# Kernel tuning notes

Measured on AMD Instinct MI355X. Metric: run time of the kernel, lower is better.

## Reference

```python
import jax, jax.numpy as jnp
import numpy as np

SLOT_DIM, EMB_DIM, HID, ACT_DIM, NUM_ACT = 256, 256, 1024, 128, 1024
EPS_SAMPLE = 1e-6
EPS_LN = 1e-5


def setup_inputs() -> dict:
    key = jax.random.key(0)
    ks = jax.random.split(key, 12)
    B, N, S = 128, 32, 12
    s = 0.02
    return {
        "slots": jax.random.normal(ks[0], (B, N, S, SLOT_DIM), jnp.float32),
        "noise": jax.random.normal(ks[1], (B, N - 1, S, ACT_DIM), jnp.float32),
        "W1": jax.random.normal(ks[2], (SLOT_DIM, HID), jnp.float32) * s,
        "b1": jnp.zeros((HID,), jnp.float32),
        "ln_g": jnp.ones((HID,), jnp.float32),
        "ln_b": jnp.zeros((HID,), jnp.float32),
        "W2": jax.random.normal(ks[3], (HID, EMB_DIM), jnp.float32) * s,
        "b2": jnp.zeros((EMB_DIM,), jnp.float32),
        "Wm": jax.random.normal(ks[4], (EMB_DIM, ACT_DIM), jnp.float32) * s,
        "bm": jnp.zeros((ACT_DIM,), jnp.float32),
        "Wv": jax.random.normal(ks[5], (EMB_DIM, ACT_DIM), jnp.float32) * s,
        "bv": jnp.zeros((ACT_DIM,), jnp.float32),
        "codebook": jax.random.normal(ks[6], (NUM_ACT, ACT_DIM), jnp.float32) * s,
    }


def reference(slots, noise, W1, b1, ln_g, ln_b, W2, b2, Wm, bm, Wv, bv, codebook):
    sg = jax.lax.stop_gradient
    B, N, S, _ = slots.shape
    # per-slot MLP encoder: Linear -> ReLU -> LayerNorm -> Linear
    h = jax.nn.relu(jnp.einsum('bnsd,dh->bnsh', slots, W1) + b1)
    mu = h.mean(-1, keepdims=True)
    var = h.var(-1, keepdims=True)
    h = (h - mu) * jax.lax.rsqrt(var + EPS_LN) * ln_g + ln_b
    e = jnp.einsum('bnsh,he->bnse', h, W2) + b2  # (B,N,S,emb)
    # action distribution from consecutive frames
    mean_tok = jnp.einsum('bnse,ea->bnsa', e, Wm) + bm
    var_tok = jnp.abs(jnp.einsum('bnse,ea->bnsa', e, Wv) + bv)
    adm = mean_tok[:, 1:] - mean_tok[:, :-1]  # (B,N-1,S,A)
    adv = var_tok[:, 1:] + var_tok[:, :-1]
    action_dist = jnp.stack([adm, adv], axis=2)  # (B,N-1,2,S,A)
    # reparameterized sample
    z = noise * jnp.sqrt(adv + EPS_SAMPLE) + adm
    # VQ: nearest codebook entry via squared L2 distances
    zf = z.reshape(-1, ACT_DIM)  # (M,A)
    d = (jnp.sum(zf * zf, axis=1, keepdims=True)
         - 2.0 * zf @ codebook.T
         + jnp.sum(codebook * codebook, axis=1))  # (M,num_actions)
    idx = jnp.argmin(d, axis=1)  # (M,)
    q = codebook[idx].reshape(z.shape)
    quant_loss = jnp.mean((sg(z) - q) ** 2)
    commit_loss = jnp.mean((z - sg(q)) ** 2)
    q_st = z + sg(q - z)  # straight-through action prototypes
    action_variability = z - sg(q)
    action_idxs = idx.reshape(B, N - 1, S, 1)
    return (action_dist, z, action_variability, q_st, action_idxs, quant_loss, commit_loss)
```

## Files before the change

kernel.cpp:

```cpp
#include <hip/hip_runtime.h>
#include <math.h>

#define HID 1024
#define SLOT 256
#define EMB 256
#define ACT 128
#define NCODE 1024
#define R_ROWS 49152
#define M_ROWS 47616

#define OFF_AD 0
#define OFF_Z  12189696
#define OFF_AV 18284544
#define OFF_QS 24379392
#define OFF_IDX 30474240
#define OFF_QL 30521856
#define OFF_CL 30521857

typedef _Float16 f16x8 __attribute__((ext_vector_type(8)));
typedef float f32x4 __attribute__((ext_vector_type(4)));

__device__ __forceinline__ void pack_body(
    const float* __restrict__ W, _Float16* __restrict__ hi, _Float16* __restrict__ lo,
    int lgS, int N, int p, const float* __restrict__ scale)
{
    int j = p & 7;
    int l = (p >> 3) & 63;
    int q = p >> 9;
    int s = q & ((1 << lgS) - 1);
    int t = q >> lgS;
    int n = t * 16 + (l & 15);
    int k = s * 32 + ((l >> 4) << 3) + j;
    float x = W[(size_t)k * N + n];
    if (scale) x *= scale[k];
    _Float16 h = (_Float16)x;
    hi[p] = h;
    lo[p] = (_Float16)(x - (float)h);
}

__global__ __launch_bounds__(256) void k_packall(
    const float* __restrict__ W1, const float* __restrict__ W2,
    const float* __restrict__ Wm, const float* __restrict__ Wv,
    const float* __restrict__ CB, const float* __restrict__ ln_g,
    const float* __restrict__ ln_b, const float* __restrict__ b2,
    _Float16* __restrict__ W1h, _Float16* __restrict__ W1l,
    _Float16* __restrict__ W2h, _Float16* __restrict__ W2l,
    _Float16* __restrict__ Wmh, _Float16* __restrict__ Wml,
    _Float16* __restrict__ Wvh, _Float16* __restrict__ Wvl,
    _Float16* __restrict__ CBh, _Float16* __restrict__ CBl,
    float* __restrict__ cn, float* __restrict__ v0, float* __restrict__ v1,
    float* __restrict__ losss)
{
    const int bi = blockIdx.x;
    const int tid = threadIdx.x;
    if (bi == 0 && tid == 0) *losss = 0.f;

    if (bi < 1024) {
        pack_body(W1, W1h, W1l, 3, HID, bi * 256 + tid, (const float*)0);
    } else if (bi < 2048) {
        pack_body(W2, W2h, W2l, 5, EMB, (bi - 1024) * 256 + tid, ln_g);
    } else if (bi < 2176) {
        pack_body(Wm, Wmh, Wml, 3, ACT, (bi - 2048) * 256 + tid, (const float*)0);
    } else if (bi < 2304) {
        pack_body(Wv, Wvh, Wvl, 3, ACT, (bi - 2176) * 256 + tid, (const float*)0);
    } else if (bi < 2816) {
        int p = (bi - 2304) * 256 + tid;
        int j = p & 7;
        int l = (p >> 3) & 63;
        int q = p >> 9;
        int s = q & 7;
        int t = q >> 3;
        int n = t * 32 + (l & 31);
        int k = s * 16 + ((l >> 5) << 3) + j;
        float x = CB[(size_t)n * ACT + k];
        _Float16 h = (_Float16)x;
        CBh[p] = h;
        CBl[p] = (_Float16)(x - (float)h);
    } else if (bi < 2820) {
        int c = (bi - 2816) * 256 + tid;
        float s = 0.f;
        #pragma unroll
        for (int k = 0; k < ACT; k += 4) {
            float4 v = *(const float4*)&CB[(size_t)c * ACT + k];
            s += v.x*v.x + v.y*v.y + v.z*v.z + v.w*v.w;
        }
        cn[c] = s;
    } else {
        int n = tid;
        float a0 = 0.f, a1 = 0.f;
        for (int c = 0; c < HID; ++c) {
            float w2 = W2[(size_t)c * EMB + n];
            a1 = fmaf(ln_g[c], w2, a1);
            a0 = fmaf(ln_b[c], w2, a0);
        }
        v1[n] = a1;
        v0[n] = a0 + b2[n];
    }
}

__global__ __launch_bounds__(512, 4) void k_gemm1(
    const float* __restrict__ X, const float* __restrict__ b1,
    const _Float16* __restrict__ W1h, const _Float16* __restrict__ W1l,
    _Float16* __restrict__ GHh, _Float16* __restrict__ GHl,
    float* __restrict__ stats, int row0)
{
    __shared__ _Float16 sh[32768];

    const int tid = threadIdx.x;
    const int w = tid >> 6, l = tid & 63, lr = l & 15, lg = l >> 4;
    const int p = blockIdx.x & 15;
    const int rg = blockIdx.x >> 4;
    const int rowc = rg * 128;

    {
        const float4* s0 = (const float4*)(W1h + (size_t)p * 16384);
        const float4* s1 = (const float4*)(W1l + (size_t)p * 16384);
        float4* d = (float4*)sh;
        #pragma unroll
        for (int i = 0; i < 4; ++i) {
            d[tid + 512 * i] = s0[tid + 512 * i];
            d[2048 + tid + 512 * i] = s1[tid + 512 * i];
        }
    }

    f16x8 a0[8], a1[8];
    {
        const float* xrow = X + (size_t)(row0 + rowc + w * 16 + lr) * SLOT + lg * 8;
        #pragma unroll
        for (int s = 0; s < 8; ++s) {
            float4 xa = *(const float4*)(xrow + 32 * s);
            float4 xb = *(const float4*)(xrow + 32 * s + 4);
            float xv[8] = {xa.x, xa.y, xa.z, xa.w, xb.x, xb.y, xb.z, xb.w};
            #pragma unroll
            for (int e = 0; e < 8; ++e) {
                _Float16 h = (_Float16)xv[e];
                a0[s][e] = h;
                a1[s][e] = (_Float16)(xv[e] - (float)h);
            }
        }
    }
    __syncthreads();

    f32x4 acc[4];
    #pragma unroll
    for (int t = 0; t < 4; ++t) acc[t] = (f32x4){0.f, 0.f, 0.f, 0.f};

    #pragma unroll
    for (int s = 0; s < 8; ++s) {
        #pragma unroll
        for (int t = 0; t < 4; ++t) {
            f16x8 bh = *(const f16x8*)&sh[((t * 8 + s) * 64 + l) * 8];
            f16x8 bl = *(const f16x8*)&sh[16384 + ((t * 8 + s) * 64 + l) * 8];
            acc[t] = __builtin_amdgcn_mfma_f32_16x16x32_f16(a0[s], bh, acc[t], 0, 0, 0);
            acc[t] = __builtin_amdgcn_mfma_f32_16x16x32_f16(a0[s], bl, acc[t], 0, 0, 0);
            acc[t] = __builtin_amdgcn_mfma_f32_16x16x32_f16(a1[s], bh, acc[t], 0, 0, 0);
        }
    }

    #pragma unroll
    for (int t = 0; t < 4; ++t) {
        float bb = b1[p * 64 + t * 16 + lr];
        #pragma unroll
        for (int r = 0; r < 4; ++r) acc[t][r] = fmaxf(acc[t][r] + bb, 0.f);
    }

    {
        float sum[4] = {0,0,0,0}, sq[4] = {0,0,0,0};
        #pragma unroll
        for (int t = 0; t < 4; ++t)
            #pragma unroll
            for (int r = 0; r < 4; ++r) {
                float v = acc[t][r];
                sum[r] += v; sq[r] = fmaf(v, v, sq[r]);
            }
        #pragma unroll
        for (int off = 1; off < 16; off <<= 1)
            #pragma unroll
            for (int r = 0; r < 4; ++r) {
                sum[r] += __shfl_xor(sum[r], off, 64);
                sq[r]  += __shfl_xor(sq[r],  off, 64);
            }
        if (lr == 0) {
            #pragma unroll
            for (int r = 0; r < 4; ++r) {
                size_t grow = (size_t)row0 + rowc + w * 16 + lg * 4 + r;
                float2 st = {sum[r], sq[r]};
                *(float2*)&stats[((size_t)p * R_ROWS + grow) * 2] = st;
            }
        }
    }
    __syncthreads();

    #pragma unroll
    for (int t = 0; t < 4; ++t) {
        #pragma unroll
        for (int r = 0; r < 4; ++r) {
            int rowloc = w * 16 + lg * 4 + r;
            int col = t * 16 + lr;
            int cc = col >> 3, j = col & 7;
            int ad = rowloc * 64 + ((cc ^ (rowloc & 7)) << 3) + j;
            float v = acc[t][r];
            _Float16 h = (_Float16)v;
            sh[ad] = h;
            sh[8192 + ad] = (_Float16)(v - (float)h);
        }
    }
    __syncthreads();

    #pragma unroll
    for (int i = 0; i < 2; ++i) {
        int u = tid + 512 * i;
        int RTl = u >> 7;
        int Sl  = (u >> 6) & 1;
        int li  = u & 63;
        int row = RTl * 16 + (li & 15);
        int cc  = Sl * 4 + (li >> 4);
        int ad  = row * 64 + ((cc ^ (row & 7)) << 3);
        f16x8 vh = *(const f16x8*)&sh[ad];
        f16x8 vl = *(const f16x8*)&sh[8192 + ad];
        size_t RTg = (size_t)rg * 8 + RTl;
        size_t off = ((RTg * 32 + (2 * p + Sl)) * 64 + li) * 8;
        *(f16x8*)&GHh[off] = vh;
        *(f16x8*)&GHl[off] = vl;
    }
}

__global__ __launch_bounds__(512, 4) void k_gemm2(
    const _Float16* __restrict__ GHh, const _Float16* __restrict__ GHl,
    const _Float16* __restrict__ W2h, const _Float16* __restrict__ W2l,
    const _Float16* __restrict__ Wmh, const _Float16* __restrict__ Wml,
    const _Float16* __restrict__ Wvh, const _Float16* __restrict__ Wvl,
    const float* __restrict__ stats, const float* __restrict__ v0,
    const float* __restrict__ v1, const float* __restrict__ bm,
    const float* __restrict__ bv,
    float* __restrict__ MT, float* __restrict__ VT, int row0)
{
    __shared__ _Float16 sh[32768];
    __shared__ float mu_s[64], rs_s[64];

    const int tid = threadIdx.x;
    const int w = tid >> 6, l = tid & 63, lr = l & 15, lg = l >> 4;
    const int rb = blockIdx.x;
    const size_t grow0 = (size_t)row0 + rb * 64;

    if (tid < 64) {
        float s = 0.f, q = 0.f;
        #pragma unroll
        for (int pp = 0; pp < 16; ++pp) {
            float2 st = *(const float2*)&stats[((size_t)pp * R_ROWS + grow0 + tid) * 2];
            s += st.x; q += st.y;
        }
        float mu = s * (1.f / HID);
        float var = q * (1.f / HID) - mu * mu;
        mu_s[tid] = mu;
        rs_s[tid] = 1.f / sqrtf(var + 1e-5f);
    }

    float v0r[2], v1r[2];
    #pragma unroll
    for (int t = 0; t < 2; ++t) {
        int n = w * 32 + t * 16 + lr;
        v0r[t] = v0[n];
        v1r[t] = v1[n];
    }

    f32x4 acc[4][2];
    #pragma unroll
    for (int rt = 0; rt < 4; ++rt)
        #pragma unroll
        for (int t = 0; t < 2; ++t) acc[rt][t] = (f32x4){0.f, 0.f, 0.f, 0.f};

    for (int kp = 0; kp < 8; ++kp) {
        __syncthreads();
        #pragma unroll
        for (int i = 0; i < 4; ++i) {
            int u = tid + 512 * i;
            int arr = u >> 10;
            int ui = u & 1023;
            int RTl = ui >> 8;
            int rem = ui & 255;
            size_t gu = ((size_t)(rb * 4 + RTl) * 32 + kp * 4) * 64 + rem;
            const _Float16* src = arr ? GHl : GHh;
            *(f16x8*)&sh[(size_t)arr * 8192 + (size_t)ui * 8] = *(const f16x8*)&src[gu * 8];
        }
        __syncthreads();

        #pragma unroll
        for (int sl = 0; sl < 4; ++sl) {
            f16x8 bh[2], bl[2];
            #pragma unroll
            for (int t = 0; t < 2; ++t) {
                int tg = w * 2 + t;
                size_t o = ((size_t)(tg * 32 + kp * 4 + sl) * 64 + l) * 8;
                bh[t] = *(const f16x8*)&W2h[o];
                bl[t] = *(const f16x8*)&W2l[o];
            }
            #pragma unroll
            for (int rt = 0; rt < 4; ++rt) {
                f16x8 ah = *(const f16x8*)&sh[((rt * 4 + sl) * 64 + l) * 8];
                f16x8 al = *(const f16x8*)&sh[8192 + ((rt * 4 + sl) * 64 + l) * 8];
                #pragma unroll
                for (int t = 0; t < 2; ++t) {
                    acc[rt][t] = __builtin_amdgcn_mfma_f32_16x16x32_f16(ah, bh[t], acc[rt][t], 0, 0, 0);
                    acc[rt][t] = __builtin_amdgcn_mfma_f32_16x16x32_f16(ah, bl[t], acc[rt][t], 0, 0, 0);
                    acc[rt][t] = __builtin_amdgcn_mfma_f32_16x16x32_f16(al, bh[t], acc[rt][t], 0, 0, 0);
                }
            }
        }
    }
    __syncthreads();

    #pragma unroll
    for (int rt = 0; rt < 4; ++rt) {
        #pragma unroll
        for (int t = 0; t < 2; ++t) {
            int n = w * 32 + t * 16 + lr;
            int cc = n >> 3, j = n & 7;
            #pragma unroll
            for (int r = 0; r < 4; ++r) {
                int row = rt * 16 + lg * 4 + r;
                float mu = mu_s[row], rs = rs_s[row];
                float e = rs * acc[rt][t][r] - rs * mu * v1r[t] + v0r[t];
                _Float16 h = (_Float16)e;
                int ad = row * 256 + ((cc ^ (row & 7)) << 3) + j;
                sh[ad] = h;
                sh[16384 + ad] = (_Float16)(e - (float)h);
            }
        }
    }
    __syncthreads();

    const _Float16* WXh = (w < 4) ? Wmh : Wvh;
    const _Float16* WXl = (w < 4) ? Wml : Wvl;
    f32x4 acc3[4][2];
    #pragma unroll
    for (int rt = 0; rt < 4; ++rt)
        #pragma unroll
        for (int t = 0; t < 2; ++t) acc3[rt][t] = (f32x4){0.f, 0.f, 0.f, 0.f};

    #pragma unroll
    for (int s = 0; s < 8; ++s) {
        f16x8 bh[2], bl[2];
        #pragma unroll
        for (int t = 0; t < 2; ++t) {
            int tg = (w & 3) * 2 + t;
            size_t o = ((size_t)(tg * 8 + s) * 64 + l) * 8;
            bh[t] = *(const f16x8*)&WXh[o];
            bl[t] = *(const f16x8*)&WXl[o];
        }
        #pragma unroll
        for (int rt = 0; rt < 4; ++rt) {
            int row = rt * 16 + lr;
            int cc = s * 4 + lg;
            int ad = row * 256 + ((cc ^ (row & 7)) << 3);
            f16x8 ah = *(const f16x8*)&sh[ad];
            f16x8 al = *(const f16x8*)&sh[16384 + ad];
            #pragma unroll
            for (int t = 0; t < 2; ++t) {
                acc3[rt][t] = __builtin_amdgcn_mfma_f32_16x16x32_f16(ah, bh[t], acc3[rt][t], 0, 0, 0);
                acc3[rt][t] = __builtin_amdgcn_mfma_f32_16x16x32_f16(ah, bl[t], acc3[rt][t], 0, 0, 0);
                acc3[rt][t] = __builtin_amdgcn_mfma_f32_16x16x32_f16(al, bh[t], acc3[rt][t], 0, 0, 0);
            }
        }
    }

    #pragma unroll
    for (int rt = 0; rt < 4; ++rt) {
        #pragma unroll
        for (int t = 0; t < 2; ++t) {
            int a = (w & 3) * 32 + t * 16 + lr;
            float bx = (w < 4) ? bm[a] : bv[a];
            #pragma unroll
            for (int r = 0; r < 4; ++r) {
                size_t grow = grow0 + rt * 16 + lg * 4 + r;
                float vv = acc3[rt][t][r] + bx;
                if (w < 4) MT[grow * ACT + a] = vv;
                else       VT[grow * ACT + a] = fabsf(vv);
            }
        }
    }
}

__global__ __launch_bounds__(256, 3) void k_vq32(
    const float* __restrict__ MT, const float* __restrict__ VT,
    const float* __restrict__ noise,
    const _Float16* __restrict__ CBh, const _Float16* __restrict__ CBl,
    const float* __restrict__ cn, const float* __restrict__ CB,
    float* __restrict__ out, float* __restrict__ losss)
{
    typedef float f32x16 __attribute__((ext_vector_type(16)));
    __shared__ _Float16 Zh[32 * 128];
    __shared__ _Float16 Zl[32 * 128];
    __shared__ float pb[4][32];
    __shared__ int   pi[4][32];
    __shared__ int   idx_s[32];
    __shared__ float red[4];

    const int tid = threadIdx.x;
    const int rowbase = blockIdx.x * 32;
    const int a = tid & 127;
    const int rhalf = tid >> 7;
    const int ga = a >> 3, ja = a & 7;

    for (int g = 0; g < 2; ++g) {
        float m1v[8], m2v[8], v1v[8], v2v[8], nzv[8];
        #pragma unroll
        for (int i = 0; i < 8; ++i) {
            int row = g * 16 + 2 * i + rhalf;
            int m = rowbase + row;
            int b = m / 372;
            int r1 = m + 12 * b;
            int r2 = r1 + 12;
            m1v[i] = MT[(size_t)r1 * ACT + a];
            m2v[i] = MT[(size_t)r2 * ACT + a];
            v1v[i] = VT[(size_t)r1 * ACT + a];
            v2v[i] = VT[(size_t)r2 * ACT + a];
            nzv[i] = noise[(size_t)m * ACT + a];
        }
        #pragma unroll
        for (int i = 0; i < 8; ++i) {
            int row = g * 16 + 2 * i + rhalf;
            int m = rowbase + row;
            float adm = m2v[i] - m1v[i];
            float adv = v2v[i] + v1v[i];
            float z = nzv[i] * sqrtf(adv + 1e-6f) + adm;
            int np = m / 12, s = m - np * 12;
            out[OFF_AD + (size_t)(np * 24 + s) * ACT + a] = adm;
            out[OFF_AD + (size_t)(np * 24 + 12 + s) * ACT + a] = adv;
            out[OFF_Z + (size_t)m * ACT + a] = z;
            _Float16 h = (_Float16)z;
            int ad = row * 128 + (((ga ^ (row & 15))) << 3) + ja;
            Zh[ad] = h;
            Zl[ad] = (_Float16)(z - (float)h);
        }
    }
    __syncthreads();

    const int w = tid >> 6, l = tid & 63;
    const int col = l & 31, hw = l >> 5;

    float best[16];
    int bidx[16];
    #pragma unroll
    for (int r = 0; r < 16; ++r) { best[r] = 3.4e38f; bidx[r] = 0; }

    for (int cc2 = 0; cc2 < 2; ++cc2) {
        f32x16 acc[4];
        #pragma unroll
        for (int t = 0; t < 4; ++t)
            #pragma unroll
            for (int r = 0; r < 16; ++r) acc[t][r] = 0.f;

        #pragma unroll
        for (int s = 0; s < 8; ++s) {
            int ad = col * 128 + (((s * 2 + hw) ^ (col & 15)) << 3);
            f16x8 ah = *(const f16x8*)&Zh[ad];
            f16x8 al = *(const f16x8*)&Zl[ad];
            #pragma unroll
            for (int t = 0; t < 4; ++t) {
                int tg = w * 8 + cc2 * 4 + t;
                f16x8 bh = *(const f16x8*)(CBh + ((size_t)(tg * 8 + s) * 64 + l) * 8);
                f16x8 bl = *(const f16x8*)(CBl + ((size_t)(tg * 8 + s) * 64 + l) * 8);
                acc[t] = __builtin_amdgcn_mfma_f32_32x32x16_f16(ah, bh, acc[t], 0, 0, 0);
                acc[t] = __builtin_amdgcn_mfma_f32_32x32x16_f16(ah, bl, acc[t], 0, 0, 0);
                acc[t] = __builtin_amdgcn_mfma_f32_32x32x16_f16(al, bh, acc[t], 0, 0, 0);
            }
        }

        float cnv[4];
        #pragma unroll
        for (int t = 0; t < 4; ++t) cnv[t] = cn[(w * 8 + cc2 * 4 + t) * 32 + col];

        #pragma unroll
        for (int reg = 0; reg < 16; ++reg) {
            #pragma unroll
            for (int t = 0; t < 4; ++t) {
                float d = cnv[t] - 2.f * acc[t][reg];
                int gi = (w * 8 + cc2 * 4 + t) * 32 + col;
                if (d < best[reg]) { best[reg] = d; bidx[reg] = gi; }
            }
        }
    }

    #pragma unroll
    for (int reg = 0; reg < 16; ++reg) {
        float bv_ = best[reg];
        int bi_ = bidx[reg];
        #pragma unroll
        for (int off = 1; off < 32; off <<= 1) {
            float ov = __shfl_xor(bv_, off, 64);
            int   oi = __shfl_xor(bi_, off, 64);
            if (ov < bv_ || (ov == bv_ && oi < bi_)) { bv_ = ov; bi_ = oi; }
        }
        if (col == 0) {
            int mrow = (reg & 3) + 8 * (reg >> 2) + 4 * hw;
            pb[w][mrow] = bv_;
            pi[w][mrow] = bi_;
        }
    }
    __syncthreads();

    if (tid < 32) {
        float bb = pb[0][tid];
        int bi_ = pi[0][tid];
        #pragma unroll
        for (int w2 = 1; w2 < 4; ++w2) {
            float v = pb[w2][tid];
            int ii = pi[w2][tid];
            if (v < bb || (v == bb && ii < bi_)) { bb = v; bi_ = ii; }
        }
        idx_s[tid] = bi_;
        out[OFF_IDX + rowbase + tid] = (float)bi_;
    }
    __syncthreads();

    float ls = 0.f;
    for (int g = 0; g < 2; ++g) {
        int civ[8]; float zv[8], qv[8];
        #pragma unroll
        for (int i = 0; i < 8; ++i) {
            int row = g * 16 + 2 * i + rhalf;
            civ[i] = idx_s[row];
            int ad = row * 128 + (((ga ^ (row & 15))) << 3) + ja;
            zv[i] = (float)Zh[ad] + (float)Zl[ad];
        }
        #pragma unroll
        for (int i = 0; i < 8; ++i) qv[i] = CB[(size_t)civ[i] * ACT + a];
        #pragma unroll
        for (int i = 0; i < 8; ++i) {
            int row = g * 16 + 2 * i + rhalf;
            size_t m = (size_t)(rowbase + row);
            float diff = zv[i] - qv[i];
            out[OFF_QS + m * ACT + a] = zv[i] + (qv[i] - zv[i]);
            out[OFF_AV + m * ACT + a] = diff;
            ls = fmaf(diff, diff, ls);
        }
    }
    #pragma unroll
    for (int off = 32; off; off >>= 1) ls += __shfl_xor(ls, off, 64);
    if (l == 0) red[w] = ls;
    __syncthreads();
    if (tid == 0) atomicAdd(losss, red[0] + red[1] + red[2] + red[3]);
}

__global__ void k_losses(const float* __restrict__ losss, float* __restrict__ out)
{
    float v = *losss * (1.f / 6094848.f);
    out[OFF_QL] = v;
    out[OFF_CL] = v;
}

extern "C" void kernel_launch(void* const* d_in, const int* in_sizes, int n_in,
                              void* d_out, int out_size, void* d_ws, size_t ws_size,
                              hipStream_t stream)
{
    const float* slots = (const float*)d_in[0];
    const float* noise = (const float*)d_in[1];
    const float* W1    = (const float*)d_in[2];
    const float* b1    = (const float*)d_in[3];
    const float* ln_g  = (const float*)d_in[4];
    const float* ln_b  = (const float*)d_in[5];
    const float* W2    = (const float*)d_in[6];
    const float* b2    = (const float*)d_in[7];
    const float* Wm    = (const float*)d_in[8];
    const float* bm    = (const float*)d_in[9];
    const float* Wv    = (const float*)d_in[10];
    const float* bv    = (const float*)d_in[11];
    const float* CB    = (const float*)d_in[12];
    float* out = (float*)d_out;
    float* ws  = (float*)d_ws;

    size_t ws_floats = ws_size / 4;
    int nchunk = (ws_floats >= 41000000) ? 2 : 4;
    int RC = R_ROWS / nchunk;

    _Float16* GHh = (_Float16*)ws;
    _Float16* GHl = (_Float16*)(ws + (size_t)RC * 512);
    float* MT = ws + (size_t)RC * 1024;
    float* VT = MT + 6291456;
    float* wb = VT + 6291456;
    _Float16* W1h = (_Float16*)(wb + 0);
    _Float16* W1l = (_Float16*)(wb + 131072);
    _Float16* W2h = (_Float16*)(wb + 262144);
    _Float16* W2l = (_Float16*)(wb + 393216);
    _Float16* Wmh = (_Float16*)(wb + 524288);
    _Float16* Wml = (_Float16*)(wb + 540672);
    _Float16* Wvh = (_Float16*)(wb + 557056);
    _Float16* Wvl = (_Float16*)(wb + 573440);
    _Float16* CBh = (_Float16*)(wb + 589824);
    _Float16* CBl = (_Float16*)(wb + 655360);
    float* cn    = wb + 720896;
    float* v0    = wb + 721920;
    float* v1    = wb + 722176;
    float* losss = wb + 722432;
    float* stats = wb + 722688;

    hipLaunchKernelGGL(k_packall, dim3(2821), dim3(256), 0, stream,
                       W1, W2, Wm, Wv, CB, ln_g, ln_b, b2,
                       W1h, W1l, W2h, W2l, Wmh, Wml, Wvh, Wvl, CBh, CBl,
                       cn, v0, v1, losss);

    for (int c = 0; c < nchunk; ++c) {
        int row0 = c * RC;
        hipLaunchKernelGGL(k_gemm1, dim3((RC / 128) * 16), dim3(512), 0, stream,
                           slots, b1, W1h, W1l, GHh, GHl, stats, row0);
        hipLaunchKernelGGL(k_gemm2, dim3(RC / 64), dim3(512), 0, stream,
                           GHh, GHl, W2h, W2l, Wmh, Wml, Wvh, Wvl,
                           stats, v0, v1, bm, bv, MT, VT, row0);
    }

    hipLaunchKernelGGL(k_vq32, dim3(M_ROWS / 32), dim3(256), 0, stream,
                       MT, VT, noise, CBh, CBl, cn, CB, out, losss);
    hipLaunchKernelGGL(k_losses, dim3(1), dim3(1), 0, stream, losss, out);
}
```

Measured before the change: 484.0 us.

## Double gemm1 row tile and retile gemm2 warps into a 2x4 grid

In k_gemm1 each block now covers 256 rows instead of 128, so every warp computes two 16-row tiles against the same shared-memory W1 slice. This reuses the staged weights across more rows and halves the grid size. Launch bounds drop to 2 blocks per SM to leave room for the doubled register footprint. In k_gemm2 the warps are rearranged into 2 row halves by 4 column groups, so each global W2 fragment load feeds 2 row tiles and each LDS A fragment feeds 4 column tiles, rebalancing global versus shared traffic. The costs are fewer blocks per chunk, lower occupancy and higher register pressure.

```diff
diff --git a/kernel.cpp b/kernel.cpp
--- a/kernel.cpp
+++ b/kernel.cpp
@@ -98,7 +98,7 @@
     }
 }
 
-__global__ __launch_bounds__(512, 4) void k_gemm1(
+__global__ __launch_bounds__(512, 2) void k_gemm1(
     const float* __restrict__ X, const float* __restrict__ b1,
     const _Float16* __restrict__ W1h, const _Float16* __restrict__ W1l,
     _Float16* __restrict__ GHh, _Float16* __restrict__ GHl,
@@ -110,7 +110,7 @@
     const int w = tid >> 6, l = tid & 63, lr = l & 15, lg = l >> 4;
     const int p = blockIdx.x & 15;
     const int rg = blockIdx.x >> 4;
-    const int rowc = rg * 128;
+    const int rowc = rg * 256;
 
     {
         const float4* s0 = (const float4*)(W1h + (size_t)p * 16384);
@@ -123,9 +123,10 @@
         }
     }
 
-    f16x8 a0[8], a1[8];
-    {
-        const float* xrow = X + (size_t)(row0 + rowc + w * 16 + lr) * SLOT + lg * 8;
+    f16x8 a0[2][8], a1[2][8];
+    #pragma unroll
+    for (int rt = 0; rt < 2; ++rt) {
+        const float* xrow = X + (size_t)(row0 + rowc + w * 32 + rt * 16 + lr) * SLOT + lg * 8;
         #pragma unroll
         for (int s = 0; s < 8; ++s) {
             float4 xa = *(const float4*)(xrow + 32 * s);
@@ -134,16 +135,18 @@
             #pragma unroll
             for (int e = 0; e < 8; ++e) {
                 _Float16 h = (_Float16)xv[e];
-                a0[s][e] = h;
-                a1[s][e] = (_Float16)(xv[e] - (float)h);
-            }
-        }
-    }
-    __syncthreads();
-
-    f32x4 acc[4];
-    #pragma unroll
-    for (int t = 0; t < 4; ++t) acc[t] = (f32x4){0.f, 0.f, 0.f, 0.f};
+                a0[rt][s][e] = h;
+                a1[rt][s][e] = (_Float16)(xv[e] - (float)h);
+            }
+        }
+    }
+    __syncthreads();
+
+    f32x4 acc[2][4];
+    #pragma unroll
+    for (int rt = 0; rt < 2; ++rt)
+        #pragma unroll
+        for (int t = 0; t < 4; ++t) acc[rt][t] = (f32x4){0.f, 0.f, 0.f, 0.f};
 
     #pragma unroll
     for (int s = 0; s < 8; ++s) {
@@ -151,26 +154,32 @@
         for (int t = 0; t < 4; ++t) {
             f16x8 bh = *(const f16x8*)&sh[((t * 8 + s) * 64 + l) * 8];
             f16x8 bl = *(const f16x8*)&sh[16384 + ((t * 8 + s) * 64 + l) * 8];
-            acc[t] = __builtin_amdgcn_mfma_f32_16x16x32_f16(a0[s], bh, acc[t], 0, 0, 0);
-            acc[t] = __builtin_amdgcn_mfma_f32_16x16x32_f16(a0[s], bl, acc[t], 0, 0, 0);
-            acc[t] = __builtin_amdgcn_mfma_f32_16x16x32_f16(a1[s], bh, acc[t], 0, 0, 0);
-        }
-    }
-
-    #pragma unroll
-    for (int t = 0; t < 4; ++t) {
-        float bb = b1[p * 64 + t * 16 + lr];
-        #pragma unroll
-        for (int r = 0; r < 4; ++r) acc[t][r] = fmaxf(acc[t][r] + bb, 0.f);
-    }
-
-    {
+            #pragma unroll
+            for (int rt = 0; rt < 2; ++rt) {
+                acc[rt][t] = __builtin_amdgcn_mfma_f32_16x16x32_f16(a0[rt][s], bh, acc[rt][t], 0, 0, 0);
+                acc[rt][t] = __builtin_amdgcn_mfma_f32_16x16x32_f16(a0[rt][s], bl, acc[rt][t], 0, 0, 0);
+                acc[rt][t] = __builtin_amdgcn_mfma_f32_16x16x32_f16(a1[rt][s], bh, acc[rt][t], 0, 0, 0);
+            }
+        }
+    }
+
+    #pragma unroll
+    for (int rt = 0; rt < 2; ++rt)
+        #pragma unroll
+        for (int t = 0; t < 4; ++t) {
+            float bb = b1[p * 64 + t * 16 + lr];
+            #pragma unroll
+            for (int r = 0; r < 4; ++r) acc[rt][t][r] = fmaxf(acc[rt][t][r] + bb, 0.f);
+        }
+
+    #pragma unroll
+    for (int rt = 0; rt < 2; ++rt) {
         float sum[4] = {0,0,0,0}, sq[4] = {0,0,0,0};
         #pragma unroll
         for (int t = 0; t < 4; ++t)
             #pragma unroll
             for (int r = 0; r < 4; ++r) {
-                float v = acc[t][r];
+                float v = acc[rt][t][r];
                 sum[r] += v; sq[r] = fmaf(v, v, sq[r]);
             }
         #pragma unroll
@@ -183,7 +192,7 @@
         if (lr == 0) {
             #pragma unroll
             for (int r = 0; r < 4; ++r) {
-                size_t grow = (size_t)row0 + rowc + w * 16 + lg * 4 + r;
+                size_t grow = (size_t)row0 + rowc + w * 32 + rt * 16 + lg * 4 + r;
                 float2 st = {sum[r], sq[r]};
                 *(float2*)&stats[((size_t)p * R_ROWS + grow) * 2] = st;
             }
@@ -192,23 +201,25 @@
     __syncthreads();
 
     #pragma unroll
-    for (int t = 0; t < 4; ++t) {
-        #pragma unroll
-        for (int r = 0; r < 4; ++r) {
-            int rowloc = w * 16 + lg * 4 + r;
-            int col = t * 16 + lr;
-            int cc = col >> 3, j = col & 7;
-            int ad = rowloc * 64 + ((cc ^ (rowloc & 7)) << 3) + j;
-            float v = acc[t][r];
-            _Float16 h = (_Float16)v;
-            sh[ad] = h;
-            sh[8192 + ad] = (_Float16)(v - (float)h);
-        }
-    }
-    __syncthreads();
-
-    #pragma unroll
-    for (int i = 0; i < 2; ++i) {
+    for (int rt = 0; rt < 2; ++rt)
+        #pragma unroll
+        for (int t = 0; t < 4; ++t) {
+            #pragma unroll
+            for (int r = 0; r < 4; ++r) {
+                int rowloc = w * 32 + rt * 16 + lg * 4 + r;
+                int col = t * 16 + lr;
+                int cc = col >> 3, j = col & 7;
+                int ad = rowloc * 64 + ((cc ^ (rowloc & 7)) << 3) + j;
+                float v = acc[rt][t][r];
+                _Float16 h = (_Float16)v;
+                sh[ad] = h;
+                sh[16384 + ad] = (_Float16)(v - (float)h);
+            }
+        }
+    __syncthreads();
+
+    #pragma unroll
+    for (int i = 0; i < 4; ++i) {
         int u = tid + 512 * i;
         int RTl = u >> 7;
         int Sl  = (u >> 6) & 1;
@@ -217,8 +228,8 @@
         int cc  = Sl * 4 + (li >> 4);
         int ad  = row * 64 + ((cc ^ (row & 7)) << 3);
         f16x8 vh = *(const f16x8*)&sh[ad];
-        f16x8 vl = *(const f16x8*)&sh[8192 + ad];
-        size_t RTg = (size_t)rg * 8 + RTl;
+        f16x8 vl = *(const f16x8*)&sh[16384 + ad];
+        size_t RTg = (size_t)rg * 16 + RTl;
         size_t off = ((RTg * 32 + (2 * p + Sl)) * 64 + li) * 8;
         *(f16x8*)&GHh[off] = vh;
         *(f16x8*)&GHl[off] = vl;
@@ -240,6 +251,7 @@
 
     const int tid = threadIdx.x;
     const int w = tid >> 6, l = tid & 63, lr = l & 15, lg = l >> 4;
+    const int rh = w >> 2, cg = w & 3;
     const int rb = blockIdx.x;
     const size_t grow0 = (size_t)row0 + rb * 64;
 
@@ -256,19 +268,19 @@
         rs_s[tid] = 1.f / sqrtf(var + 1e-5f);
     }
 
-    float v0r[2], v1r[2];
-    #pragma unroll
-    for (int t = 0; t < 2; ++t) {
-        int n = w * 32 + t * 16 + lr;
+    float v0r[4], v1r[4];
+    #pragma unroll
+    for (int t = 0; t < 4; ++t) {
+        int n = cg * 64 + t * 16 + lr;
         v0r[t] = v0[n];
         v1r[t] = v1[n];
     }
 
-    f32x4 acc[4][2];
-    #pragma unroll
-    for (int rt = 0; rt < 4; ++rt)
-        #pragma unroll
-        for (int t = 0; t < 2; ++t) acc[rt][t] = (f32x4){0.f, 0.f, 0.f, 0.f};
+    f32x4 acc[2][4];
+    #pragma unroll
+    for (int rt = 0; rt < 2; ++rt)
+        #pragma unroll
+        for (int t = 0; t < 4; ++t) acc[rt][t] = (f32x4){0.f, 0.f, 0.f, 0.f};
 
     for (int kp = 0; kp < 8; ++kp) {
         __syncthreads();
@@ -287,20 +299,21 @@
 
         #pragma unroll
         for (int sl = 0; sl < 4; ++sl) {
-            f16x8 bh[2], bl[2];
-            #pragma unroll
-            for (int t = 0; t < 2; ++t) {
-                int tg = w * 2 + t;
+            f16x8 bh[4], bl[4];
+            #pragma unroll
+            for (int t = 0; t < 4; ++t) {
+                int tg = cg * 4 + t;
                 size_t o = ((size_t)(tg * 32 + kp * 4 + sl) * 64 + l) * 8;
                 bh[t] = *(const f16x8*)&W2h[o];
                 bl[t] = *(const f16x8*)&W2l[o];
             }
             #pragma unroll
-            for (int rt = 0; rt < 4; ++rt) {
-                f16x8 ah = *(const f16x8*)&sh[((rt * 4 + sl) * 64 + l) * 8];
-                f16x8 al = *(const f16x8*)&sh[8192 + ((rt * 4 + sl) * 64 + l) * 8];
+            for (int rt = 0; rt < 2; ++rt) {
+                int RT = rh * 2 + rt;
+                f16x8 ah = *(const f16x8*)&sh[((RT * 4 + sl) * 64 + l) * 8];
+                f16x8 al = *(const f16x8*)&sh[8192 + ((RT * 4 + sl) * 64 + l) * 8];
                 #pragma unroll
-                for (int t = 0; t < 2; ++t) {
+                for (int t = 0; t < 4; ++t) {
                     acc[rt][t] = __builtin_amdgcn_mfma_f32_16x16x32_f16(ah, bh[t], acc[rt][t], 0, 0, 0);
                     acc[rt][t] = __builtin_amdgcn_mfma_f32_16x16x32_f16(ah, bl[t], acc[rt][t], 0, 0, 0);
                     acc[rt][t] = __builtin_amdgcn_mfma_f32_16x16x32_f16(al, bh[t], acc[rt][t], 0, 0, 0);
@@ -311,14 +324,14 @@
     __syncthreads();
 
     #pragma unroll
-    for (int rt = 0; rt < 4; ++rt) {
-        #pragma unroll
-        for (int t = 0; t < 2; ++t) {
-            int n = w * 32 + t * 16 + lr;
+    for (int rt = 0; rt < 2; ++rt) {
+        #pragma unroll
+        for (int t = 0; t < 4; ++t) {
+            int n = cg * 64 + t * 16 + lr;
             int cc = n >> 3, j = n & 7;
             #pragma unroll
             for (int r = 0; r < 4; ++r) {
-                int row = rt * 16 + lg * 4 + r;
+                int row = rh * 32 + rt * 16 + lg * 4 + r;
                 float mu = mu_s[row], rs = rs_s[row];
                 float e = rs * acc[rt][t][r] - rs * mu * v1r[t] + v0r[t];
                 _Float16 h = (_Float16)e;
@@ -602,7 +615,7 @@
 
     for (int c = 0; c < nchunk; ++c) {
         int row0 = c * RC;
-        hipLaunchKernelGGL(k_gemm1, dim3((RC / 128) * 16), dim3(512), 0, stream,
+        hipLaunchKernelGGL(k_gemm1, dim3((RC / 256) * 16), dim3(512), 0, stream,
                            slots, b1, W1h, W1l, GHh, GHl, stats, row0);
         hipLaunchKernelGGL(k_gemm2, dim3(RC / 64), dim3(512), 0, stream,
                            GHh, GHl, W2h, W2l, Wmh, Wml, Wvh, Wvl,
```

Measured after the change: 557.5 us. 1.15x slower.
